# Optimization experiments

Hardware: AMD Instinct MI355X
Metric: run time of the kernel (lower is better)

## Reference

```python
import jax, jax.numpy as jnp
import numpy as np

B, N, M, DIM, H, DH = 2, 2048, 2048, 512, 8, 64
INNER = H * DH  # 512


def setup_inputs() -> dict:
    key = jax.random.key(0)
    ks = jax.random.split(key, 9)
    s = 0.02
    return {
        "x": jax.random.normal(ks[0], (B, N, DIM), jnp.float32),
        "x1": jax.random.normal(ks[1], (B, M, DIM), jnp.float32),
        "attn_mat": jax.random.normal(ks[2], (B, H, N, M), jnp.float32),
        "dots_para": jax.random.uniform(ks[3], (1,), jnp.float32),
        "mat_para": jax.random.uniform(ks[4], (1,), jnp.float32),
        "W_qv": jax.random.normal(ks[5], (DIM, 2 * INNER), jnp.float32) * s,
        "W_k": jax.random.normal(ks[6], (DIM, INNER), jnp.float32) * s,
        "W_out": jax.random.normal(ks[7], (INNER, DIM), jnp.float32) * s,
        "b_out": jax.random.normal(ks[8], (DIM,), jnp.float32) * s,
    }


def _split_heads(t):
    # [b, n, h*d] -> [b, h, n, d]
    b, n, _ = t.shape
    return t.reshape(b, n, H, DH).transpose(0, 2, 1, 3)


def reference(x, x1, attn_mat, dots_para, mat_para, W_qv, W_k, W_out, b_out):
    scale = DH ** -0.5
    qv = x @ W_qv                      # [b, n, 2*inner]
    q, v = jnp.split(qv, 2, axis=-1)
    q = _split_heads(q)                # [b, h, n, d]
    v = _split_heads(v)                # [b, h, n, d]
    k = _split_heads(x1 @ W_k)         # [b, h, m, d]
    dots = jnp.einsum("bhnd,bhmd->bhnm", q, k) * scale
    dots = dots * dots_para + attn_mat * mat_para
    attn = jax.nn.softmax(dots, axis=-1)
    out = jnp.einsum("bhnm,bhmd->bhnd", attn, v)
    out = out.transpose(0, 2, 1, 3).reshape(x.shape[0], x.shape[1], INNER)
    return out @ W_out + b_out
```

## Files before the change

kernel.cpp:

```cpp
#include <hip/hip_runtime.h>
#include <hip/hip_bf16.h>

#define NB 2048
#define MB 2048
#define SPLITS 4
#define MSP (MB / SPLITS)

typedef __attribute__((ext_vector_type(8))) short short8;
typedef __attribute__((ext_vector_type(4))) float floatx4;

__device__ __forceinline__ unsigned short f2bf(float f) {
    union { float f; unsigned int u; } v; v.f = f;
    unsigned int r = (v.u + 0x7FFFu + ((v.u >> 16) & 1u)) >> 16;
    return (unsigned short)r;
}

__device__ __forceinline__ int swz(int row, int k) {
    return (row << 6) + ((((k >> 3) ^ (row & 7))) << 3) + (k & 7);
}

__launch_bounds__(256)
__global__ void prep(const float* __restrict__ x, const float* __restrict__ x1,
                     const float* __restrict__ Wqv, const float* __restrict__ Wk,
                     const float* __restrict__ Wout,
                     unsigned short* __restrict__ xb, unsigned short* __restrict__ x1b,
                     unsigned short* __restrict__ Wqvt, unsigned short* __restrict__ Wkt,
                     unsigned short* __restrict__ Woutt) {
    __shared__ float t[64][65];
    const int bid = blockIdx.x, tid = threadIdx.x;
    if (bid < 2048) {
        const float* in = bid < 1024 ? x : x1;
        unsigned short* out = bid < 1024 ? xb : x1b;
        size_t off = ((size_t)(bid & 1023) * 256 + tid) * 8;
        float4 d0 = *(const float4*)(in + off);
        float4 d1 = *(const float4*)(in + off + 4);
        uint4 o;
        o.x = (unsigned int)f2bf(d0.x) | ((unsigned int)f2bf(d0.y) << 16);
        o.y = (unsigned int)f2bf(d0.z) | ((unsigned int)f2bf(d0.w) << 16);
        o.z = (unsigned int)f2bf(d1.x) | ((unsigned int)f2bf(d1.y) << 16);
        o.w = (unsigned int)f2bf(d1.z) | ((unsigned int)f2bf(d1.w) << 16);
        *(uint4*)(out + off) = o;
        return;
    }
    int tb = bid - 2048;
    const float* W; unsigned short* Wt; int N;
    if (tb < 128)      { W = Wqv;  Wt = Wqvt;  N = 1024; }
    else if (tb < 192) { tb -= 128; W = Wk;   Wt = Wkt;   N = 512; }
    else               { tb -= 192; W = Wout; Wt = Woutt; N = 512; }
    const int k0 = (tb & 7) * 64, n0 = (tb >> 3) * 64;
#pragma unroll
    for (int p = 0; p < 4; p++) {
        int idx = p * 256 + tid;
        int kr = idx >> 4, c4 = (idx & 15) << 2;
        float4 d = *(const float4*)(W + (size_t)(k0 + kr) * N + n0 + c4);
        t[kr][c4 + 0] = d.x; t[kr][c4 + 1] = d.y; t[kr][c4 + 2] = d.z; t[kr][c4 + 3] = d.w;
    }
    __syncthreads();
#pragma unroll
    for (int p = 0; p < 4; p++) {
        int idx = p * 256 + tid;
        int nr = idx >> 4, k4 = (idx & 15) << 2;
        uint2 o;
        o.x = (unsigned int)f2bf(t[k4 + 0][nr]) | ((unsigned int)f2bf(t[k4 + 1][nr]) << 16);
        o.y = (unsigned int)f2bf(t[k4 + 2][nr]) | ((unsigned int)f2bf(t[k4 + 3][nr]) << 16);
        *(uint2*)(Wt + (size_t)(n0 + nr) * 512 + k0 + k4) = o;
    }
}

template <int MODE>
__device__ __forceinline__ void gemm64_body(const unsigned short* __restrict__ A,
                                            const unsigned short* __restrict__ Bt,
                                            const float* __restrict__ bias,
                                            void* __restrict__ Cp, int Nc, int m0, int n0,
                                            short* Al, short* Bl) {
    const int tid = threadIdx.x;
    const int w = tid >> 6, lane = tid & 63;
    const int quad = lane >> 4, c16 = lane & 15;
    const int wr = (w >> 1) * 32, wc = (w & 1) * 32;

    floatx4 acc[2][2];
#pragma unroll
    for (int i = 0; i < 2; i++)
#pragma unroll
        for (int j = 0; j < 2; j++) acc[i][j] = floatx4{0.f, 0.f, 0.f, 0.f};

    for (int kk = 0; kk < 512; kk += 64) {
        __syncthreads();
#pragma unroll
        for (int p = 0; p < 2; p++) {
            int id = p * 256 + tid;
            int row = id >> 3, c8 = (id & 7) << 3;
            *(uint4*)&Al[swz(row, c8)] = *(const uint4*)(A + (size_t)(m0 + row) * 512 + kk + c8);
            *(uint4*)&Bl[swz(row, c8)] = *(const uint4*)(Bt + (size_t)(n0 + row) * 512 + kk + c8);
        }
        __syncthreads();
#pragma unroll
        for (int kc = 0; kc < 2; kc++) {
            short8 af[2], bf[2];
#pragma unroll
            for (int mt = 0; mt < 2; mt++)
                af[mt] = *(const short8*)&Al[swz(wr + mt * 16 + c16, kc * 32 + quad * 8)];
#pragma unroll
            for (int nt = 0; nt < 2; nt++)
                bf[nt] = *(const short8*)&Bl[swz(wc + nt * 16 + c16, kc * 32 + quad * 8)];
#pragma unroll
            for (int mt = 0; mt < 2; mt++)
#pragma unroll
                for (int nt = 0; nt < 2; nt++)
                    acc[mt][nt] = __builtin_amdgcn_mfma_f32_16x16x32_bf16(af[mt], bf[nt], acc[mt][nt], 0, 0, 0);
        }
    }
#pragma unroll
    for (int mt = 0; mt < 2; mt++)
#pragma unroll
        for (int nt = 0; nt < 2; nt++) {
            if (MODE == 2) {
                int col2 = n0 + wc + nt * 16 + c16 - 512;
                int hh = col2 >> 6, dd = col2 & 63;
                int row0 = m0 + wr + mt * 16 + quad * 4;
                int bb = row0 >> 11, nb = row0 & 2047;
                uint2 o;
                o.x = (unsigned int)f2bf(acc[mt][nt][0]) | ((unsigned int)f2bf(acc[mt][nt][1]) << 16);
                o.y = (unsigned int)f2bf(acc[mt][nt][2]) | ((unsigned int)f2bf(acc[mt][nt][3]) << 16);
                *(uint2*)((unsigned short*)Cp + ((size_t)((bb * 8 + hh) * 64 + dd)) * 2048 + nb) = o;
            } else {
#pragma unroll
                for (int r = 0; r < 4; r++) {
                    int row = m0 + wr + mt * 16 + quad * 4 + r;
                    int col = n0 + wc + nt * 16 + c16;
                    float v = acc[mt][nt][r];
                    if (MODE == 1) {
                        ((unsigned short*)Cp)[(size_t)row * Nc + col] = f2bf(v);
                    } else {
                        ((float*)Cp)[(size_t)row * Nc + col] = v + bias[col];
                    }
                }
            }
        }
}

__launch_bounds__(256)
__global__ void gemm_qvk(const unsigned short* __restrict__ xb, const unsigned short* __restrict__ x1b,
                         const unsigned short* __restrict__ Wqvt, const unsigned short* __restrict__ Wkt,
                         unsigned short* __restrict__ qvbf, unsigned short* __restrict__ vt,
                         unsigned short* __restrict__ kbf) {
    __shared__ short Al[64 * 64];
    __shared__ short Bl[64 * 64];
    int bid = blockIdx.x;
    if (bid < 1024) {
        int m0 = (bid & 63) * 64, n0 = (bid >> 6) * 64;
        if (n0 < 512)
            gemm64_body<1>(xb, Wqvt, nullptr, qvbf, 1024, m0, n0, Al, Bl);
        else
            gemm64_body<2>(xb, Wqvt, nullptr, vt, 1024, m0, n0, Al, Bl);
    } else {
        bid -= 1024;
        gemm64_body<1>(x1b, Wkt, nullptr, kbf, 512, (bid & 63) * 64, (bid >> 6) * 64, Al, Bl);
    }
}

__launch_bounds__(256)
__global__ void gemm_out(const unsigned short* __restrict__ A, const unsigned short* __restrict__ Bt,
                         const float* __restrict__ bias, float* __restrict__ C) {
    __shared__ short Al[64 * 64];
    __shared__ short Bl[64 * 64];
    gemm64_body<0>(A, Bt, bias, C, 512, blockIdx.x * 64, blockIdx.y * 64, Al, Bl);
}

__launch_bounds__(256)
__global__ void flash_attn(const unsigned short* __restrict__ qv,
                           const unsigned short* __restrict__ kb,
                           const unsigned short* __restrict__ vt,
                           const float* __restrict__ attn_mat,
                           const float* __restrict__ dots_para,
                           const float* __restrict__ mat_para,
                           float* __restrict__ Opart,
                           float* __restrict__ lpart) {
    __shared__ short QP[4][32 * 64];
    __shared__ short Ks[2][64 * 64];
    __shared__ short Vs[2][64 * 64];

    const int tid = threadIdx.x, w = tid >> 6, lane = tid & 63;
    const int quad = lane >> 4, c16 = lane & 15;
    const int q0 = blockIdx.x * 128;
    const int bh = blockIdx.y;
    const int sp = blockIdx.z;
    const int b = bh >> 3, h = bh & 7;
    const int ms = sp * MSP;

    const float log2e = 1.4426950408889634f;
    const float mp = mat_para[0] * log2e;
    const float sdp = dots_para[0] * 0.125f * log2e;

    short* QPf = (short*)QP;
#pragma unroll
    for (int p = 0; p < 4; p++) {
        int id = p * 256 + tid;
        int r = id >> 3, c = id & 7;
        *(uint4*)&QPf[swz(r, c * 8)] =
            *(const uint4*)(qv + (size_t)(b * NB + q0 + r) * 1024 + h * 64 + c * 8);
    }
    __syncthreads();
    short8 qf[2][2];
#pragma unroll
    for (int at = 0; at < 2; at++)
#pragma unroll
        for (int kc = 0; kc < 2; kc++)
            qf[at][kc] = *(const short8*)&QPf[swz(w * 32 + at * 16 + c16, kc * 32 + quad * 8)];
    short* Pw = &QPf[w * 2048];

    const int sr = tid >> 3, sc = tid & 7;
    const unsigned short* vbase = vt + (size_t)((b * 8 + h) * 64) * 2048;
    uint4 kreg[2], vreg[2];
    auto loadKV = [&](int m) {
#pragma unroll
        for (int p = 0; p < 2; p++) {
            int r = p * 32 + sr;
            kreg[p] = *(const uint4*)(kb + (size_t)(b * MB + m + r) * 512 + h * 64 + sc * 8);
            vreg[p] = *(const uint4*)(vbase + (size_t)r * 2048 + m + sc * 8);
        }
    };
    auto storeKV = [&](int bufi) {
#pragma unroll
        for (int p = 0; p < 2; p++) {
            int r = p * 32 + sr;
            *(uint4*)&Ks[bufi][swz(r, sc * 8)] = kreg[p];
            *(uint4*)&Vs[bufi][swz(r, sc * 8)] = vreg[p];
        }
    };
    const float* amp = attn_mat + ((size_t)bh * NB + q0 + w * 32 + quad * 4) * MB + c16;
    float amr[2][4][4];
    auto loadAM = [&](int m0_) {
#pragma unroll
        for (int at = 0; at < 2; at++)
#pragma unroll
            for (int r = 0; r < 4; r++)
#pragma unroll
                for (int t = 0; t < 4; t++)
                    amr[at][t][r] = amp[(size_t)(at * 16 + r) * MB + m0_ + t * 16];
    };

    loadKV(ms);
    storeKV(0);
    loadKV(ms + 64);
    loadAM(ms);

    floatx4 O[2][4];
    float l[2][4];
#pragma unroll
    for (int at = 0; at < 2; at++)
#pragma unroll
        for (int i = 0; i < 4; i++) { O[at][i] = floatx4{0.f, 0.f, 0.f, 0.f}; l[at][i] = 0.f; }

    for (int it = 0; it < MSP / 64; it++) {
        const int m0 = ms + it * 64;
        const int buf = it & 1, nbuf = buf ^ 1;
        __syncthreads();
        storeKV(nbuf);
        int mnn = m0 + 128; if (mnn >= ms + MSP) mnn = ms;
        loadKV(mnn);

        floatx4 S[2][4];
#pragma unroll
        for (int t = 0; t < 4; t++) {
            short8 kf0 = *(const short8*)&Ks[buf][swz(t * 16 + c16, quad * 8)];
            short8 kf1 = *(const short8*)&Ks[buf][swz(t * 16 + c16, 32 + quad * 8)];
#pragma unroll
            for (int at = 0; at < 2; at++) {
                floatx4 s = floatx4{0.f, 0.f, 0.f, 0.f};
                s = __builtin_amdgcn_mfma_f32_16x16x32_bf16(qf[at][0], kf0, s, 0, 0, 0);
                s = __builtin_amdgcn_mfma_f32_16x16x32_bf16(qf[at][1], kf1, s, 0, 0, 0);
                S[at][t] = s;
            }
        }

#pragma unroll
        for (int at = 0; at < 2; at++)
#pragma unroll
            for (int t = 0; t < 4; t++)
#pragma unroll
                for (int r = 0; r < 4; r++) {
                    float p = exp2f(fmaf(S[at][t][r], sdp, amr[at][t][r] * mp));
                    l[at][r] += p;
                    Pw[swz(at * 16 + quad * 4 + r, t * 16 + c16)] = (short)f2bf(p);
                }
        int mnx = m0 + 64; if (mnx >= ms + MSP) mnx = ms;
        loadAM(mnx);
        __threadfence_block();

        short8 pf[2][2];
#pragma unroll
        for (int at = 0; at < 2; at++)
#pragma unroll
            for (int kc = 0; kc < 2; kc++)
                pf[at][kc] = *(const short8*)&Pw[swz(at * 16 + c16, kc * 32 + quad * 8)];
#pragma unroll
        for (int dt = 0; dt < 4; dt++) {
            short8 vf0 = *(const short8*)&Vs[buf][swz(dt * 16 + c16, quad * 8)];
            short8 vf1 = *(const short8*)&Vs[buf][swz(dt * 16 + c16, 32 + quad * 8)];
#pragma unroll
            for (int at = 0; at < 2; at++) {
                O[at][dt] = __builtin_amdgcn_mfma_f32_16x16x32_bf16(pf[at][0], vf0, O[at][dt], 0, 0, 0);
                O[at][dt] = __builtin_amdgcn_mfma_f32_16x16x32_bf16(pf[at][1], vf1, O[at][dt], 0, 0, 0);
            }
        }
    }

#pragma unroll
    for (int at = 0; at < 2; at++) {
#pragma unroll
        for (int r = 0; r < 4; r++) {
            float s = l[at][r];
            s += __shfl_xor(s, 1);
            s += __shfl_xor(s, 2);
            s += __shfl_xor(s, 4);
            s += __shfl_xor(s, 8);
            l[at][r] = s;
        }
        if (c16 == 0) {
#pragma unroll
            for (int r = 0; r < 4; r++)
                lpart[(size_t)(sp * 16 + bh) * NB + q0 + w * 32 + at * 16 + quad * 4 + r] = l[at][r];
        }
#pragma unroll
        for (int dt = 0; dt < 4; dt++)
#pragma unroll
            for (int r = 0; r < 4; r++) {
                size_t row = (size_t)sp * 4096 + b * NB + q0 + w * 32 + at * 16 + quad * 4 + r;
                Opart[row * 512 + h * 64 + dt * 16 + c16] = O[at][dt][r];
            }
    }
}

__launch_bounds__(256)
__global__ void combine_splits(const float* __restrict__ Opart, const float* __restrict__ lpart,
                               unsigned short* __restrict__ ao) {
    int idx = blockIdx.x * 256 + threadIdx.x;
    int row = idx >> 7;
    int col = (idx & 127) << 2;
    int b = row >> 11, n = row & 2047, h = col >> 6;
    float ls = 0.f;
    float4 o = {0.f, 0.f, 0.f, 0.f};
#pragma unroll
    for (int sp = 0; sp < SPLITS; sp++) {
        ls += lpart[(size_t)(sp * 16 + b * 8 + h) * NB + n];
        float4 os = *(const float4*)(Opart + ((size_t)sp * 4096 + row) * 512 + col);
        o.x += os.x; o.y += os.y; o.z += os.z; o.w += os.w;
    }
    float rinv = 1.0f / ls;
    uint2 pk;
    pk.x = (unsigned int)f2bf(o.x * rinv) | ((unsigned int)f2bf(o.y * rinv) << 16);
    pk.y = (unsigned int)f2bf(o.z * rinv) | ((unsigned int)f2bf(o.w * rinv) << 16);
    *(uint2*)(ao + (size_t)row * 512 + col) = pk;
}

extern "C" void kernel_launch(void* const* d_in, const int* in_sizes, int n_in,
                              void* d_out, int out_size, void* d_ws, size_t ws_size,
                              hipStream_t stream) {
    const float* x         = (const float*)d_in[0];
    const float* x1        = (const float*)d_in[1];
    const float* attn_mat  = (const float*)d_in[2];
    const float* dots_para = (const float*)d_in[3];
    const float* mat_para  = (const float*)d_in[4];
    const float* W_qv      = (const float*)d_in[5];
    const float* W_k       = (const float*)d_in[6];
    const float* W_out     = (const float*)d_in[7];
    const float* b_out     = (const float*)d_in[8];
    float* out = (float*)d_out;

    unsigned short* xb    = (unsigned short*)d_ws;
    unsigned short* x1b   = xb    + (size_t)4096 * 512;
    unsigned short* qvbf  = x1b   + (size_t)4096 * 512;
    unsigned short* vt    = qvbf  + (size_t)4096 * 1024;
    unsigned short* kbf   = vt    + (size_t)2 * 8 * 64 * 2048;
    unsigned short* aobf  = kbf   + (size_t)4096 * 512;
    unsigned short* Wqvt  = aobf  + (size_t)4096 * 512;
    unsigned short* Wkt   = Wqvt  + (size_t)1024 * 512;
    unsigned short* Woutt = Wkt   + (size_t)512 * 512;
    float*          Opart = (float*)(Woutt + (size_t)512 * 512);
    float*          lpart = Opart + (size_t)SPLITS * 4096 * 512;

    dim3 blk(256);
    prep<<<2304, blk, 0, stream>>>(x, x1, W_qv, W_k, W_out, xb, x1b, Wqvt, Wkt, Woutt);
    gemm_qvk<<<1536, blk, 0, stream>>>(xb, x1b, Wqvt, Wkt, qvbf, vt, kbf);
    flash_attn<<<dim3(16, 16, SPLITS), blk, 0, stream>>>(qvbf, kbf, vt, attn_mat, dots_para, mat_para,
                                                         Opart, lpart);
    combine_splits<<<2048, blk, 0, stream>>>(Opart, lpart, aobf);
    gemm_out<<<dim3(64, 8), blk, 0, stream>>>(aobf, Woutt, b_out, out);
}
```

Before: 464.0 us.

## Fuse fp32-to-bf16 input cast into QVK GEMM and use three attention splits

Removes the separate activation conversion pass in prep: the QVK GEMM now loads fp32 x/x1 directly and packs to bf16 while staging to LDS, avoiding a bf16 round-trip through global memory. Flash attention changes from 4 key splits to 3 uneven splits (11/11/10 tiles of 64) to change grid size and reduce partial-output traffic in combine. bf16 packing switches to the hardware packed conversion intrinsic. The GEMM loads now read twice the bytes of A per tile, and the uneven split gives one workgroup less work than the others.

```diff
diff --git a/kernel.cpp b/kernel.cpp
--- a/kernel.cpp
+++ b/kernel.cpp
@@ -3,8 +3,7 @@
 
 #define NB 2048
 #define MB 2048
-#define SPLITS 4
-#define MSP (MB / SPLITS)
+#define SPLITS 3
 
 typedef __attribute__((ext_vector_type(8))) short short8;
 typedef __attribute__((ext_vector_type(4))) float floatx4;
@@ -14,35 +13,23 @@
     unsigned int r = (v.u + 0x7FFFu + ((v.u >> 16) & 1u)) >> 16;
     return (unsigned short)r;
 }
+__device__ __forceinline__ unsigned int pk2bf(float a, float b) {
+    __hip_bfloat162 h = __float22bfloat162_rn(float2{a, b});
+    return *(unsigned int*)&h;
+}
 
 __device__ __forceinline__ int swz(int row, int k) {
     return (row << 6) + ((((k >> 3) ^ (row & 7))) << 3) + (k & 7);
 }
 
 __launch_bounds__(256)
-__global__ void prep(const float* __restrict__ x, const float* __restrict__ x1,
-                     const float* __restrict__ Wqv, const float* __restrict__ Wk,
+__global__ void prep(const float* __restrict__ Wqv, const float* __restrict__ Wk,
                      const float* __restrict__ Wout,
-                     unsigned short* __restrict__ xb, unsigned short* __restrict__ x1b,
                      unsigned short* __restrict__ Wqvt, unsigned short* __restrict__ Wkt,
                      unsigned short* __restrict__ Woutt) {
     __shared__ float t[64][65];
-    const int bid = blockIdx.x, tid = threadIdx.x;
-    if (bid < 2048) {
-        const float* in = bid < 1024 ? x : x1;
-        unsigned short* out = bid < 1024 ? xb : x1b;
-        size_t off = ((size_t)(bid & 1023) * 256 + tid) * 8;
-        float4 d0 = *(const float4*)(in + off);
-        float4 d1 = *(const float4*)(in + off + 4);
-        uint4 o;
-        o.x = (unsigned int)f2bf(d0.x) | ((unsigned int)f2bf(d0.y) << 16);
-        o.y = (unsigned int)f2bf(d0.z) | ((unsigned int)f2bf(d0.w) << 16);
-        o.z = (unsigned int)f2bf(d1.x) | ((unsigned int)f2bf(d1.y) << 16);
-        o.w = (unsigned int)f2bf(d1.z) | ((unsigned int)f2bf(d1.w) << 16);
-        *(uint4*)(out + off) = o;
-        return;
-    }
-    int tb = bid - 2048;
+    int tb = blockIdx.x;
+    const int tid = threadIdx.x;
     const float* W; unsigned short* Wt; int N;
     if (tb < 128)      { W = Wqv;  Wt = Wqvt;  N = 1024; }
     else if (tb < 192) { tb -= 128; W = Wk;   Wt = Wkt;   N = 512; }
@@ -61,14 +48,14 @@
         int idx = p * 256 + tid;
         int nr = idx >> 4, k4 = (idx & 15) << 2;
         uint2 o;
-        o.x = (unsigned int)f2bf(t[k4 + 0][nr]) | ((unsigned int)f2bf(t[k4 + 1][nr]) << 16);
-        o.y = (unsigned int)f2bf(t[k4 + 2][nr]) | ((unsigned int)f2bf(t[k4 + 3][nr]) << 16);
+        o.x = pk2bf(t[k4 + 0][nr], t[k4 + 1][nr]);
+        o.y = pk2bf(t[k4 + 2][nr], t[k4 + 3][nr]);
         *(uint2*)(Wt + (size_t)(n0 + nr) * 512 + k0 + k4) = o;
     }
 }
 
-template <int MODE>
-__device__ __forceinline__ void gemm64_body(const unsigned short* __restrict__ A,
+template <int MODE, int AF32>
+__device__ __forceinline__ void gemm64_body(const void* __restrict__ Ap,
                                             const unsigned short* __restrict__ Bt,
                                             const float* __restrict__ bias,
                                             void* __restrict__ Cp, int Nc, int m0, int n0,
@@ -90,7 +77,17 @@
         for (int p = 0; p < 2; p++) {
             int id = p * 256 + tid;
             int row = id >> 3, c8 = (id & 7) << 3;
-            *(uint4*)&Al[swz(row, c8)] = *(const uint4*)(A + (size_t)(m0 + row) * 512 + kk + c8);
+            uint4 a;
+            if (AF32) {
+                const float* Af = (const float*)Ap + (size_t)(m0 + row) * 512 + kk + c8;
+                float4 d0 = *(const float4*)Af;
+                float4 d1 = *(const float4*)(Af + 4);
+                a.x = pk2bf(d0.x, d0.y); a.y = pk2bf(d0.z, d0.w);
+                a.z = pk2bf(d1.x, d1.y); a.w = pk2bf(d1.z, d1.w);
+            } else {
+                a = *(const uint4*)((const unsigned short*)Ap + (size_t)(m0 + row) * 512 + kk + c8);
+            }
+            *(uint4*)&Al[swz(row, c8)] = a;
             *(uint4*)&Bl[swz(row, c8)] = *(const uint4*)(Bt + (size_t)(n0 + row) * 512 + kk + c8);
         }
         __syncthreads();
@@ -120,8 +117,8 @@
                 int row0 = m0 + wr + mt * 16 + quad * 4;
                 int bb = row0 >> 11, nb = row0 & 2047;
                 uint2 o;
-                o.x = (unsigned int)f2bf(acc[mt][nt][0]) | ((unsigned int)f2bf(acc[mt][nt][1]) << 16);
-                o.y = (unsigned int)f2bf(acc[mt][nt][2]) | ((unsigned int)f2bf(acc[mt][nt][3]) << 16);
+                o.x = pk2bf(acc[mt][nt][0], acc[mt][nt][1]);
+                o.y = pk2bf(acc[mt][nt][2], acc[mt][nt][3]);
                 *(uint2*)((unsigned short*)Cp + ((size_t)((bb * 8 + hh) * 64 + dd)) * 2048 + nb) = o;
             } else {
 #pragma unroll
@@ -140,7 +137,7 @@
 }
 
 __launch_bounds__(256)
-__global__ void gemm_qvk(const unsigned short* __restrict__ xb, const unsigned short* __restrict__ x1b,
+__global__ void gemm_qvk(const float* __restrict__ x, const float* __restrict__ x1,
                          const unsigned short* __restrict__ Wqvt, const unsigned short* __restrict__ Wkt,
                          unsigned short* __restrict__ qvbf, unsigned short* __restrict__ vt,
                          unsigned short* __restrict__ kbf) {
@@ -150,12 +147,12 @@
     if (bid < 1024) {
         int m0 = (bid & 63) * 64, n0 = (bid >> 6) * 64;
         if (n0 < 512)
-            gemm64_body<1>(xb, Wqvt, nullptr, qvbf, 1024, m0, n0, Al, Bl);
+            gemm64_body<1, 1>(x, Wqvt, nullptr, qvbf, 1024, m0, n0, Al, Bl);
         else
-            gemm64_body<2>(xb, Wqvt, nullptr, vt, 1024, m0, n0, Al, Bl);
+            gemm64_body<2, 1>(x, Wqvt, nullptr, vt, 1024, m0, n0, Al, Bl);
     } else {
         bid -= 1024;
-        gemm64_body<1>(x1b, Wkt, nullptr, kbf, 512, (bid & 63) * 64, (bid >> 6) * 64, Al, Bl);
+        gemm64_body<1, 1>(x1, Wkt, nullptr, kbf, 512, (bid & 63) * 64, (bid >> 6) * 64, Al, Bl);
     }
 }
 
@@ -164,7 +161,7 @@
                          const float* __restrict__ bias, float* __restrict__ C) {
     __shared__ short Al[64 * 64];
     __shared__ short Bl[64 * 64];
-    gemm64_body<0>(A, Bt, bias, C, 512, blockIdx.x * 64, blockIdx.y * 64, Al, Bl);
+    gemm64_body<0, 0>(A, Bt, bias, C, 512, blockIdx.x * 64, blockIdx.y * 64, Al, Bl);
 }
 
 __launch_bounds__(256)
@@ -186,7 +183,9 @@
     const int bh = blockIdx.y;
     const int sp = blockIdx.z;
     const int b = bh >> 3, h = bh & 7;
-    const int ms = sp * MSP;
+    const int t0 = sp * 11;
+    const int ntl = (sp == 2) ? 10 : 11;
+    const int ms = t0 * 64;
 
     const float log2e = 1.4426950408889634f;
     const float mp = mat_para[0] * log2e;
@@ -252,13 +251,12 @@
 #pragma unroll
         for (int i = 0; i < 4; i++) { O[at][i] = floatx4{0.f, 0.f, 0.f, 0.f}; l[at][i] = 0.f; }
 
-    for (int it = 0; it < MSP / 64; it++) {
-        const int m0 = ms + it * 64;
+    for (int it = 0; it < ntl; it++) {
         const int buf = it & 1, nbuf = buf ^ 1;
         __syncthreads();
         storeKV(nbuf);
-        int mnn = m0 + 128; if (mnn >= ms + MSP) mnn = ms;
-        loadKV(mnn);
+        int i2 = it + 2;
+        loadKV((i2 < ntl ? t0 + i2 : t0) * 64);
 
         floatx4 S[2][4];
 #pragma unroll
@@ -284,8 +282,8 @@
                     l[at][r] += p;
                     Pw[swz(at * 16 + quad * 4 + r, t * 16 + c16)] = (short)f2bf(p);
                 }
-        int mnx = m0 + 64; if (mnx >= ms + MSP) mnx = ms;
-        loadAM(mnx);
+        int i1 = it + 1;
+        loadAM((i1 < ntl ? t0 + i1 : t0) * 64);
         __threadfence_block();
 
         short8 pf[2][2];
@@ -349,8 +347,8 @@
     }
     float rinv = 1.0f / ls;
     uint2 pk;
-    pk.x = (unsigned int)f2bf(o.x * rinv) | ((unsigned int)f2bf(o.y * rinv) << 16);
-    pk.y = (unsigned int)f2bf(o.z * rinv) | ((unsigned int)f2bf(o.w * rinv) << 16);
+    pk.x = pk2bf(o.x * rinv, o.y * rinv);
+    pk.y = pk2bf(o.z * rinv, o.w * rinv);
     *(uint2*)(ao + (size_t)row * 512 + col) = pk;
 }
 
@@ -368,9 +366,7 @@
     const float* b_out     = (const float*)d_in[8];
     float* out = (float*)d_out;
 
-    unsigned short* xb    = (unsigned short*)d_ws;
-    unsigned short* x1b   = xb    + (size_t)4096 * 512;
-    unsigned short* qvbf  = x1b   + (size_t)4096 * 512;
+    unsigned short* qvbf  = (unsigned short*)d_ws;
     unsigned short* vt    = qvbf  + (size_t)4096 * 1024;
     unsigned short* kbf   = vt    + (size_t)2 * 8 * 64 * 2048;
     unsigned short* aobf  = kbf   + (size_t)4096 * 512;
@@ -381,8 +377,8 @@
     float*          lpart = Opart + (size_t)SPLITS * 4096 * 512;
 
     dim3 blk(256);
-    prep<<<2304, blk, 0, stream>>>(x, x1, W_qv, W_k, W_out, xb, x1b, Wqvt, Wkt, Woutt);
-    gemm_qvk<<<1536, blk, 0, stream>>>(xb, x1b, Wqvt, Wkt, qvbf, vt, kbf);
+    prep<<<256, blk, 0, stream>>>(W_qv, W_k, W_out, Wqvt, Wkt, Woutt);
+    gemm_qvk<<<1536, blk, 0, stream>>>(x, x1, Wqvt, Wkt, qvbf, vt, kbf);
     flash_attn<<<dim3(16, 16, SPLITS), blk, 0, stream>>>(qvbf, kbf, vt, attn_mat, dots_para, mat_para,
                                                          Opart, lpart);
     combine_splits<<<2048, blk, 0, stream>>>(Opart, lpart, aobf);
```

After: 466.3 us. Within noise of the previous version (+0.5%).
